# Performance work log

Measured on AMD Instinct MI355X. Metric: run time of the kernel, lower is better.

The kernel has to match this reference:

```python
import jax, jax.numpy as jnp
import numpy as np

N_EMBED = 1024
N_HEAD = 16
HEAD_SIZE = N_EMBED // N_HEAD  # 64
SEQ = 2048
BATCH = 2
EPS = 1e-5


def setup_inputs() -> dict:
    key = jax.random.key(0)
    ks = jax.random.split(key, 16)
    s = lambda fan_in: 1.0 / np.sqrt(fan_in)
    d, h, hs, f = N_EMBED, N_HEAD, HEAD_SIZE, 4 * N_EMBED
    return {
        "x": jax.random.normal(ks[0], (BATCH, SEQ, d), dtype=jnp.float32),
        # per-head QKV projections (no bias), stacked over heads: [H, D, hs]
        "wq": jax.random.normal(ks[1], (h, d, hs), dtype=jnp.float32) * s(d),
        "wk": jax.random.normal(ks[2], (h, d, hs), dtype=jnp.float32) * s(d),
        "wv": jax.random.normal(ks[3], (h, d, hs), dtype=jnp.float32) * s(d),
        "w_proj": jax.random.normal(ks[4], (d, d), dtype=jnp.float32) * s(d),
        "b_proj": jnp.zeros((d,), dtype=jnp.float32),
        "w1": jax.random.normal(ks[5], (d, f), dtype=jnp.float32) * s(d),
        "b1": jnp.zeros((f,), dtype=jnp.float32),
        "w2": jax.random.normal(ks[6], (f, d), dtype=jnp.float32) * s(f),
        "b2": jnp.zeros((d,), dtype=jnp.float32),
        "g1": jnp.ones((d,), dtype=jnp.float32),
        "be1": jnp.zeros((d,), dtype=jnp.float32),
        "g2": jnp.ones((d,), dtype=jnp.float32),
        "be2": jnp.zeros((d,), dtype=jnp.float32),
    }


def _layer_norm(x, gamma, beta):
    mu = jnp.mean(x, axis=-1, keepdims=True)
    var = jnp.mean(jnp.square(x - mu), axis=-1, keepdims=True)
    return (x - mu) * jax.lax.rsqrt(var + EPS) * gamma + beta


def reference(x, wq, wk, wv, w_proj, b_proj, w1, b1, w2, b2, g1, be1, g2, be2):
    B, S, D = x.shape
    # per-head projections (vectorized over heads): [B, H, S, hs]
    q = jnp.einsum("bsd,hdk->bhsk", x, wq)
    k = jnp.einsum("bsd,hdk->bhsk", x, wk)
    v = jnp.einsum("bsd,hdk->bhsk", x, wv)
    scale = HEAD_SIZE ** -0.5
    scores = jnp.einsum("bhsk,bhtk->bhst", q, k) * scale  # [B,H,S,S]
    causal = jnp.tril(jnp.ones((S, S), dtype=bool))
    scores = jnp.where(causal, scores, -jnp.inf)
    w = jax.nn.softmax(scores, axis=-1)  # dropout=0 -> identity
    attn = jnp.einsum("bhst,bhtk->bhsk", w, v)  # [B,H,S,hs]
    # concat heads (head-major ordering matches torch.cat over heads)
    attn = attn.transpose(0, 2, 1, 3).reshape(B, S, D)
    y = attn @ w_proj + b_proj
    x = _layer_norm(x + y, g1, be1)
    y = jax.nn.relu(x @ w1 + b1) @ w2 + b2
    x = _layer_norm(x + y, g2, be2)
    return x
```

## Files before the change

kernel.cpp:

```cpp
#include <hip/hip_runtime.h>


typedef unsigned short u16;
typedef unsigned int u32;
typedef __attribute__((ext_vector_type(8))) short bf16x8;
typedef __attribute__((ext_vector_type(4))) float f32x4;
typedef __attribute__((ext_vector_type(2))) u32 u32x2;
typedef __attribute__((ext_vector_type(4))) _Float16 f16x4;

#define MFMA16(a, b, c) __builtin_amdgcn_mfma_f32_16x16x32_bf16(a, b, c, 0, 0, 0)
#define MFMAH(a, b, c) __builtin_amdgcn_mfma_f32_16x16x16f16(a, b, c, 0, 0, 0)

__device__ __forceinline__ u16 f2b(float f) {
  unsigned int u = __builtin_bit_cast(unsigned int, f);
  u = (u + 0x7fffu + ((u >> 16) & 1u)) >> 16;
  return (u16)u;
}

__device__ __forceinline__ void gload_lds16(const u16* g, u16* l) {
  __builtin_amdgcn_global_load_lds((const __attribute__((address_space(1))) void*)g,
                                   (__attribute__((address_space(3))) void*)l, 16, 0, 0);
}

__device__ __forceinline__ u32 pkrtz(float lo, float hi) {
  return __builtin_bit_cast(u32, __builtin_amdgcn_cvt_pkrtz(lo, hi));
}

__device__ __forceinline__ f16x4 pack4h(float a, float b, float c, float d) {
  u32x2 r = {pkrtz(a, b), pkrtz(c, d)};
  return __builtin_bit_cast(f16x4, r);
}

__device__ __forceinline__ u16 f2h(float v) {
  return __builtin_bit_cast(u16, (_Float16)v);
}


__global__ __launch_bounds__(256) void pack_all(
    const float* __restrict__ x, const float* __restrict__ wq,
    const float* __restrict__ wk, const float* __restrict__ wv,
    const float* __restrict__ wp, const float* __restrict__ w1,
    const float* __restrict__ w2, u16* __restrict__ Xbf, u16* __restrict__ WqkvT,
    u16* __restrict__ WprojT, u16* __restrict__ W1T, u16* __restrict__ W2T) {
  int bid = blockIdx.x;
  int t = threadIdx.x;
  if (bid >= 12288) {
    size_t i = ((size_t)(bid - 12288) * 256 + t) * 4;
    float4 v = *(const float4*)(x + i);
    Xbf[i + 0] = f2b(v.x);
    Xbf[i + 1] = f2b(v.y);
    Xbf[i + 2] = f2b(v.z);
    Xbf[i + 3] = f2b(v.w);
    return;
  }
  __shared__ float tile[32][33];
  int tx = t & 31, ty = t >> 5;
  const float* src;
  u16* dst;
  int R, C, r0, c0;
  float scale = 1.0f;
  if (bid < 3072) {
    int z = bid >> 6, q = bid & 63;
    int p = z >> 4, h = z & 15;
    src = (p == 0 ? wq : (p == 1 ? wk : wv)) + (size_t)h * 1024 * 64;
    scale = (p == 0) ? 0.1803368801f : 1.0f;
    dst = WqkvT + (size_t)(p * 1024 + h * 64) * 1024;
    R = 1024; C = 64;
    c0 = (q & 1) * 32; r0 = (q >> 1) * 32;
  } else if (bid < 4096) {
    int q = bid - 3072;
    src = wp; dst = WprojT; R = 1024; C = 1024;
    c0 = (q & 31) * 32; r0 = (q >> 5) * 32;
  } else if (bid < 8192) {
    int q = bid - 4096;
    src = w1; dst = W1T; R = 1024; C = 4096;
    c0 = (q & 127) * 32; r0 = (q >> 7) * 32;
  } else {
    int q = bid - 8192;
    src = w2; dst = W2T; R = 4096; C = 1024;
    c0 = (q & 31) * 32; r0 = (q >> 5) * 32;
  }
#pragma unroll
  for (int i = 0; i < 4; ++i)
    tile[ty + i * 8][tx] = src[(size_t)(r0 + ty + i * 8) * C + c0 + tx];
  __syncthreads();
#pragma unroll
  for (int i = 0; i < 4; ++i)
    dst[(size_t)(c0 + ty + i * 8) * R + r0 + tx] = f2b(tile[tx][ty + i * 8] * scale);
}


template <int MODE>
__global__ __launch_bounds__(256, 4) void gemm_bf16(const u16* __restrict__ A,
                                                    const u16* __restrict__ Bt, int M,
                                                    int N, int Kc, int lda,
                                                    const float* __restrict__ bias,
                                                    u16* __restrict__ outB, int ldc,
                                                    u16* __restrict__ vtg) {
  constexpr int BM = 128, BN = 128, BK = 64;
  constexpr int IM = 4, JN = 4;
  __shared__ u16 As[BM * BK];
  __shared__ u16 Bs[BN * BK];
  int t = threadIdx.x;
  int m0 = blockIdx.x * BM, n0 = blockIdx.y * BN;
  int kb = blockIdx.z * Kc;
  int lane = t & 63, wid = t >> 6;
  int wm = (wid >> 1) * 64, wn = (wid & 1) * 64;
  int m16 = lane & 15, quad = lane >> 4;
  int sw = m16 & 7;

  f32x4 acc[IM][JN] = {};

  for (int k0 = kb; k0 < kb + Kc; k0 += BK) {
    __syncthreads();
#pragma unroll
    for (int i = 0; i < 4; ++i) {
      int S = i * 256 + t;
      int row = S >> 3, c = S & 7;
      gload_lds16(&A[(size_t)(m0 + row) * lda + k0 + (c ^ (row & 7)) * 8],
                  &As[(i * 256 + wid * 64) * 8]);
    }
#pragma unroll
    for (int i = 0; i < 4; ++i) {
      int S = i * 256 + t;
      int row = S >> 3, c = S & 7;
      gload_lds16(&Bt[(size_t)(n0 + row) * lda + k0 + (c ^ (row & 7)) * 8],
                  &Bs[(i * 256 + wid * 64) * 8]);
    }
    __syncthreads();
#pragma unroll
    for (int kk = 0; kk < 2; ++kk) {
      bf16x8 af[IM], bfr[JN];
      int slot = (kk * 4 + quad) ^ sw;
#pragma unroll
      for (int i = 0; i < IM; ++i)
        af[i] = *(const bf16x8*)&As[(wm + i * 16 + m16) * BK + slot * 8];
#pragma unroll
      for (int j = 0; j < JN; ++j)
        bfr[j] = *(const bf16x8*)&Bs[(wn + j * 16 + m16) * BK + slot * 8];
#pragma unroll
      for (int i = 0; i < IM; ++i)
#pragma unroll
        for (int j = 0; j < JN; ++j) acc[i][j] = MFMA16(af[i], bfr[j], acc[i][j]);
    }
  }

  if (MODE == 3 && n0 >= 2048) {
#pragma unroll
    for (int i = 0; i < IM; ++i)
#pragma unroll
      for (int j = 0; j < JN; ++j) {
        int dg = n0 + wn + j * 16 + m16 - 2048;
        int hh = dg >> 6, dd = dg & 63;
        int token = m0 + wm + i * 16 + quad * 4;
        int bb = token >> 11, tt = token & 2047;
        u32x2 pv = {pkrtz(acc[i][j][0], acc[i][j][1]),
                    pkrtz(acc[i][j][2], acc[i][j][3])};
        *(u32x2*)&vtg[(((size_t)bb * 16 + hh) * 64 + dd) * 2048 + tt] = pv;
      }
    return;
  }

  u16* pb = (MODE == 4) ? outB + (size_t)blockIdx.z * M * N : outB;
#pragma unroll
  for (int i = 0; i < IM; ++i)
#pragma unroll
    for (int j = 0; j < JN; ++j) {
      int col = n0 + wn + j * 16 + m16;
      float bv = (MODE == 1) ? bias[col] : 0.0f;
#pragma unroll
      for (int r = 0; r < 4; ++r) {
        int row = m0 + wm + i * 16 + quad * 4 + r;
        float v = acc[i][j][r];
        if (MODE == 1) {
          v += bv;
          v = v > 0.0f ? v : 0.0f;
          pb[(size_t)row * ldc + col] = f2b(v);
        } else if (MODE == 4) {
          pb[(size_t)row * ldc + col] = f2h(v);
        } else {
          pb[(size_t)row * ldc + col] = f2b(v);
        }
      }
    }
}


template <int MODE>
__global__ __launch_bounds__(512) void gemm8(const u16* __restrict__ A,
                                             const u16* __restrict__ Bt, int M, int N,
                                             int Kc, int lda,
                                             const float* __restrict__ bias,
                                             u16* __restrict__ outB, int ldc) {
  __shared__ __align__(16) u16 As[2][2][128 * 64];
  __shared__ __align__(16) u16 Bs[2][2][128 * 64];
  int t = threadIdx.x;
  int lane = t & 63, wid = t >> 6;
  int m16 = lane & 15, quad = lane >> 4, sw = m16 & 7;
  int wr = wid >> 2, wc = wid & 3;
  int m0 = blockIdx.x * 256, n0 = blockIdx.y * 256;
  int kb = blockIdx.z * Kc;
  int NT = Kc >> 6;

  int ahalf = t >> 8;
  int at = t & 255;
  int aw = wid & 3;
  int brow0 = (wc & 1) * 64;

  f32x4 acc[8][4] = {};
  bf16x8 afc[2][2], afn[2][2], bfc[4][2], bfn[4][2];

#define STAGE_B(bf, bh, kt)                                                        \
  {                                                                                \
    _Pragma("unroll") for (int l = 0; l < 2; ++l) {                                \
      int slot = l * 512 + t;                                                      \
      int row = slot >> 3, c = slot & 7;                                           \
      gload_lds16(&Bt[(size_t)(n0 + (bh)*128 + row) * lda + kb + (kt)*64 +         \
                      (c ^ (row & 7)) * 8],                                        \
                  &Bs[bf][bh][(l * 512 + wid * 64) * 8]);                          \
    }                                                                              \
  }

#define STAGE_A(bf, qp, kt)                                                        \
  {                                                                                \
    _Pragma("unroll") for (int l = 0; l < 2; ++l) {                                \
      int slot = l * 256 + at;                                                     \
      int row = slot >> 3, c = slot & 7;                                           \
      int lrow = (qp)*64 + row;                                                    \
      gload_lds16(&A[(size_t)(m0 + ahalf * 128 + lrow) * lda + kb + (kt)*64 +      \
                     (c ^ (row & 7)) * 8],                                         \
                  &As[bf][ahalf][((qp)*512 + l * 256 + aw * 64) * 8]);             \
    }                                                                              \
  }

#define READ_AF(dst, base, qdv)                                                    \
  {                                                                                \
    _Pragma("unroll") for (int mi = 0; mi < 2; ++mi)                               \
        _Pragma("unroll") for (int kk = 0; kk < 2; ++kk)                           \
            dst[mi][kk] = *(const bf16x8*)&(base)[((qdv)*32 + mi * 16 + m16) * 64 +\
                                                  ((kk * 4 + quad) ^ sw) * 8];     \
  }

#define READ_BF(dst, base)                                                         \
  {                                                                                \
    _Pragma("unroll") for (int j = 0; j < 4; ++j)                                  \
        _Pragma("unroll") for (int kk = 0; kk < 2; ++kk)                           \
            dst[j][kk] = *(const bf16x8*)&(base)[(brow0 + j * 16 + m16) * 64 +     \
                                                 ((kk * 4 + quad) ^ sw) * 8];      \
  }

  STAGE_B(0, 0, 0);
  STAGE_B(0, 1, 0);
  STAGE_A(0, 0, 0);
  STAGE_A(0, 1, 0);
  if (NT > 1) {
    STAGE_B(1, 0, 1);
    STAGE_B(1, 1, 1);
    STAGE_A(1, 0, 1);
    asm volatile("s_waitcnt vmcnt(6)" ::: "memory");
  } else {
    asm volatile("s_waitcnt vmcnt(0)" ::: "memory");
  }
  __builtin_amdgcn_s_barrier();
  asm volatile("" ::: "memory");
  READ_BF(bfc, &Bs[0][wc >> 1][0]);
  READ_AF(afc, &As[0][wr][0], 0);

  for (int kt = 0; kt < NT; ++kt) {
    int buf = kt & 1;
    const u16* Ab = &As[buf][wr][0];
    const u16* Abn = &As[buf ^ 1][wr][0];
    const u16* Bbn = &Bs[buf ^ 1][wc >> 1][0];
#pragma unroll
    for (int qd = 0; qd < 4; ++qd) {
      if (qd < 3) {
        READ_AF(afn, Ab, qd + 1);
      } else if (kt + 1 < NT) {
        READ_BF(bfn, Bbn);
        READ_AF(afn, Abn, 0);
      }
      if (qd == 0) {
        if (kt + 1 < NT) STAGE_A(buf ^ 1, 1, kt + 1);
      } else if (qd == 1) {
        if (kt + 2 < NT) STAGE_B(buf, 0, kt + 2);
      } else if (qd == 2) {
        if (kt + 2 < NT) STAGE_B(buf, 1, kt + 2);
      } else {
        if (kt + 2 < NT) STAGE_A(buf, 0, kt + 2);
      }
      if (qd < 3)
        asm volatile("s_waitcnt lgkmcnt(4)" ::: "memory");
      else if (kt + 1 < NT)
        asm volatile("s_waitcnt lgkmcnt(12)" ::: "memory");
      else
        asm volatile("s_waitcnt lgkmcnt(0)" ::: "memory");
      __builtin_amdgcn_sched_barrier(0);
      __builtin_amdgcn_s_setprio(1);
#pragma unroll
      for (int mi = 0; mi < 2; ++mi)
#pragma unroll
        for (int j = 0; j < 4; ++j)
#pragma unroll
          for (int kk = 0; kk < 2; ++kk)
            acc[qd * 2 + mi][j] = MFMA16(afc[mi][kk], bfc[j][kk], acc[qd * 2 + mi][j]);
      __builtin_amdgcn_s_setprio(0);
      if (qd == 0) {
        if (kt + 1 < NT)
          asm volatile("s_waitcnt vmcnt(8)" ::: "memory");
        else
          asm volatile("s_waitcnt vmcnt(0)" ::: "memory");
      } else if (qd == 2) {
        if (kt + 2 < NT)
          asm volatile("s_waitcnt vmcnt(6)" ::: "memory");
        else
          asm volatile("s_waitcnt vmcnt(0)" ::: "memory");
      }
      if (qd < 3 || kt + 1 < NT) {
#pragma unroll
        for (int mi = 0; mi < 2; ++mi)
#pragma unroll
          for (int kk = 0; kk < 2; ++kk) afc[mi][kk] = afn[mi][kk];
        if (qd == 3) {
#pragma unroll
          for (int j = 0; j < 4; ++j)
#pragma unroll
            for (int kk = 0; kk < 2; ++kk) bfc[j][kk] = bfn[j][kk];
        }
      }
      asm volatile("" ::: "memory");
      __builtin_amdgcn_s_barrier();
      asm volatile("" ::: "memory");
    }
  }

  u16* pb = (MODE == 4) ? outB + (size_t)blockIdx.z * M * N : outB;
#pragma unroll
  for (int mf = 0; mf < 8; ++mf)
#pragma unroll
    for (int j = 0; j < 4; ++j) {
      int col = n0 + wc * 64 + j * 16 + m16;
      float bv = (MODE == 1) ? bias[col] : 0.0f;
#pragma unroll
      for (int r = 0; r < 4; ++r) {
        int row = m0 + wr * 128 + mf * 16 + quad * 4 + r;
        float v = acc[mf][j][r];
        if (MODE == 1) {
          v += bv;
          v = v > 0.0f ? v : 0.0f;
          pb[(size_t)row * ldc + col] = f2b(v);
        } else {
          pb[(size_t)row * ldc + col] = f2h(v);
        }
      }
    }
#undef STAGE_B
#undef STAGE_A
#undef READ_AF
#undef READ_BF
}


__constant__ unsigned char R_QB[40] = {
    15, 15, 15, 15, 14, 14, 11, 11, 11, 10, 7,  7,  3,
    14, 14, 13, 13, 13, 13, 12, 12, 10, 10, 9,  9,  6,  6,
    12, 12, 9,  8,  8,  8,  5,  5,  2,
    4,  4,  1,  0};
__constant__ unsigned char R_K0[40] = {
    0,  8,  16, 24, 0,  8,  0,  8,  16, 0,  0,  8,  0,
    16, 23, 0,  7,  14, 21, 0,  7,  8,  15, 0,  7,  0,  7,
    14, 20, 14, 0,  6,  12, 0,  6,  0,
    0,  5,  0,  0};
__constant__ unsigned char R_NIT[40] = {
    8, 8, 8, 8, 8, 8, 8, 8, 8, 8, 8, 8, 8,
    7, 7, 7, 7, 7, 7, 7, 7, 7, 7, 7, 7, 7, 7,
    6, 6, 6, 6, 6, 6, 6, 6, 6,
    5, 5, 4, 2};
__constant__ unsigned char R_ST[40] = {
    32, 33, 34, 35, 28, 29, 17, 18, 19, 14, 6,  7,  255,
    30, 31, 24, 25, 26, 27, 20, 21, 15, 16, 11, 12, 4,  5,
    22, 23, 13, 8,  9,  10, 2,  3,  255,
    0,  1,  255, 255};
__constant__ unsigned char CB_BASE[12] = {0, 2, 4, 6, 8, 11, 14, 17, 20, 24, 28, 32};

__global__ __launch_bounds__(256) void attn_part(const u16* __restrict__ qk,
                                                 const u16* __restrict__ vtg,
                                                 u16* __restrict__ attn_out,
                                                 u16* __restrict__ opart0,
                                                 u16* __restrict__ opart1,
                                                 float2* __restrict__ ml) {
  int rank = blockIdx.x >> 5, bh = blockIdx.x & 31;
  int qb = R_QB[rank];
  int k_start = R_K0[rank] * 64;
  int iters = R_NIT[rank];
  int st = R_ST[rank];
  int b = bh >> 4, h = bh & 15;

  int t = threadIdx.x, lane = t & 63, w = t >> 6;
  int m16 = lane & 15, quad = lane >> 4;
  int wq0 = qb * 128 + w * 32;

  __shared__ u16 Ks[2][64 * 64];
  __shared__ u16 Vs[2][64 * 64];

  bf16x8 qa[2][2];
#pragma unroll
  for (int qs = 0; qs < 2; ++qs) {
    const u16* qp = qk + (size_t)(b * 2048 + wq0 + qs * 16 + m16) * 2048 + h * 64;
    qa[qs][0] = *(const bf16x8*)&qp[quad * 8];
    qa[qs][1] = *(const bf16x8*)&qp[32 + quad * 8];
  }

  f32x4 oT[2][4] = {};
  f32x4 oL[2] = {};
  const f16x4 ones = {(_Float16)1.0f, (_Float16)1.0f, (_Float16)1.0f, (_Float16)1.0f};

  int row0 = t >> 3, c0 = t & 7;
  int row1 = 32 + row0;
  const u16* kbase = qk + (size_t)(b * 2048) * 2048 + 1024 + h * 64;
  const u16* vbase = vtg + ((size_t)(b * 16 + h) * 64) * 2048;
  int sw = m16 & 7;

#define STAGE_ASYNC(T0, BUF)                                                        \
  {                                                                                 \
    gload_lds16(&kbase[(size_t)((T0) + row0) * 2048 + (c0 ^ (row0 & 7)) * 8],       \
                &Ks[BUF][(w * 64) * 8]);                                            \
    gload_lds16(&kbase[(size_t)((T0) + row1) * 2048 + (c0 ^ (row1 & 7)) * 8],       \
                &Ks[BUF][(256 + w * 64) * 8]);                                      \
    gload_lds16(&vbase[(size_t)row0 * 2048 + (T0) + (c0 ^ (row0 & 7)) * 8],         \
                &Vs[BUF][(w * 64) * 8]);                                            \
    gload_lds16(&vbase[(size_t)row1 * 2048 + (T0) + (c0 ^ (row1 & 7)) * 8],         \
                &Vs[BUF][(256 + w * 64) * 8]);                                      \
  }

  STAGE_ASYNC(k_start, 0);
  __syncthreads();

  for (int it = 0; it < iters; ++it) {
    int t0 = k_start + it * 64;
    int cur = it & 1;
    if (it + 1 < iters) STAGE_ASYNC(t0 + 64, !cur);

    if (t0 <= wq0 + 31) {
      f32x4 sv[2][4];
      __builtin_amdgcn_s_setprio(1);
#pragma unroll
      for (int ts = 0; ts < 4; ++ts) {
        bf16x8 ka0 = *(const bf16x8*)&Ks[cur][(ts * 16 + m16) * 64 + (quad ^ sw) * 8];
        bf16x8 ka1 =
            *(const bf16x8*)&Ks[cur][(ts * 16 + m16) * 64 + ((4 + quad) ^ sw) * 8];
#pragma unroll
        for (int qs = 0; qs < 2; ++qs) {
          f32x4 a = {};
          a = MFMA16(ka0, qa[qs][0], a);
          a = MFMA16(ka1, qa[qs][1], a);
          sv[qs][ts] = a;
        }
      }
      __builtin_amdgcn_s_setprio(0);
      if (t0 + 63 > wq0) {
#pragma unroll
        for (int qs = 0; qs < 2; ++qs)
#pragma unroll
          for (int ts = 0; ts < 4; ++ts)
#pragma unroll
            for (int rr = 0; rr < 4; ++rr) {
              int key = t0 + ts * 16 + quad * 4 + rr;
              if (key > wq0 + qs * 16 + m16) sv[qs][ts][rr] = -3e38f;
            }
      }
      f16x4 pf[2][4];
#pragma unroll
      for (int qs = 0; qs < 2; ++qs)
#pragma unroll
        for (int ts = 0; ts < 4; ++ts) {
          float p0 = exp2f(sv[qs][ts][0] - 8.0f);
          float p1 = exp2f(sv[qs][ts][1] - 8.0f);
          float p2 = exp2f(sv[qs][ts][2] - 8.0f);
          float p3 = exp2f(sv[qs][ts][3] - 8.0f);
          pf[qs][ts] = pack4h(p0, p1, p2, p3);
        }
      __builtin_amdgcn_s_setprio(1);
#pragma unroll
      for (int ts = 0; ts < 4; ++ts) {
        oL[0] = MFMAH(ones, pf[0][ts], oL[0]);
        oL[1] = MFMAH(ones, pf[1][ts], oL[1]);
#pragma unroll
        for (int ds = 0; ds < 4; ++ds) {
          f16x4 av = __builtin_bit_cast(
              f16x4, *(const u32x2*)&Vs[cur][(ds * 16 + m16) * 64 +
                                             (((ts * 2 + (quad >> 1)) ^ sw) * 8) +
                                             (quad & 1) * 4]);
          oT[0][ds] = MFMAH(av, pf[0][ts], oT[0][ds]);
          oT[1][ds] = MFMAH(av, pf[1][ts], oT[1][ds]);
        }
      }
      __builtin_amdgcn_s_setprio(0);
    }
    __syncthreads();
  }
#undef STAGE_ASYNC

  if (st == 255) {
#pragma unroll
    for (int qs = 0; qs < 2; ++qs) {
      float rl = 1.0f / oL[qs][0];
      int q = wq0 + qs * 16 + m16;
#pragma unroll
      for (int ds = 0; ds < 4; ++ds) {
        f32x4 o = oT[qs][ds];
        u32x2 ov = {(u32)f2b(o[0] * rl) | ((u32)f2b(o[1] * rl) << 16),
                    (u32)f2b(o[2] * rl) | ((u32)f2b(o[3] * rl) << 16)};
        *(u32x2*)&attn_out[(size_t)(b * 2048 + q) * 1024 + h * 64 + ds * 16 +
                           quad * 4] = ov;
      }
    }
  } else {
    u16* po;
    size_t sb;
    if (st < 32) {
      po = opart0;
      sb = ((size_t)st * 32 + bh) * 128;
    } else {
      po = opart1;
      sb = ((size_t)(st - 32) * 32 + bh) * 128;
    }
    size_t mlb = ((size_t)st * 32 + bh) * 128;
#pragma unroll
    for (int qs = 0; qs < 2; ++qs) {
      float ls = oL[qs][0];
      int qloc = w * 32 + qs * 16 + m16;
#pragma unroll
      for (int ds = 0; ds < 4; ++ds) {
        f32x4 o = oT[qs][ds];
        u32x2 ov = {pkrtz(o[0], o[1]), pkrtz(o[2], o[3])};
        *(u32x2*)&po[(sb + qloc) * 64 + ds * 16 + quad * 4] = ov;
      }
      if (quad == 0) ml[mlb + qloc] = make_float2(0.0f, ls);
    }
  }
}

__global__ __launch_bounds__(256) void attn_comb(const u16* __restrict__ opart0,
                                                 const u16* __restrict__ opart1,
                                                 const float2* __restrict__ ml,
                                                 u16* __restrict__ attn_out) {
  int qb = 4 + blockIdx.x, bh = blockIdx.y;
  int b = bh >> 4, h = bh & 15;
  int nseg = (qb < 8) ? 2 : (qb < 12 ? 3 : 4);
  int base = CB_BASE[qb - 4];
  int t = threadIdx.x;
  int q = t >> 1, dh = (t & 1) * 32;

  float lsum = 0.0f;
  for (int s = 0; s < nseg; ++s)
    lsum += ml[((size_t)(base + s) * 32 + bh) * 128 + q].y;
  float rl = 1.0f / lsum;

  constexpr size_t SLOT = (size_t)32 * 128 * 64;
  const u16* orow[4];
  for (int s = 0; s < nseg; ++s) {
    int sa = base + s;
    const u16* bp =
        (sa < 32) ? opart0 + (size_t)sa * SLOT : opart1 + (size_t)(sa - 32) * SLOT;
    orow[s] = bp + ((size_t)bh * 128 + q) * 64 + dh;
  }

  size_t oout = (size_t)(b * 2048 + qb * 128 + q) * 1024 + h * 64 + dh;
#pragma unroll 2
  for (int dd = 0; dd < 32; dd += 4) {
    float o0 = 0, o1 = 0, o2 = 0, o3 = 0;
    for (int s = 0; s < nseg; ++s) {
      f16x4 hv = __builtin_bit_cast(f16x4, *(const u32x2*)&orow[s][dd]);
      o0 += (float)hv[0];
      o1 += (float)hv[1];
      o2 += (float)hv[2];
      o3 += (float)hv[3];
    }
    u32x2 ov = {(u32)f2b(o0 * rl) | ((u32)f2b(o1 * rl) << 16),
                (u32)f2b(o2 * rl) | ((u32)f2b(o3 * rl) << 16)};
    *(u32x2*)&attn_out[oout + dd] = ov;
  }
}


__global__ __launch_bounds__(256) void ln_comb(const u16* __restrict__ parts, int np,
                                               const float* __restrict__ bias,
                                               const float* __restrict__ resid,
                                               const float* __restrict__ g,
                                               const float* __restrict__ be,
                                               float* __restrict__ outF,
                                               u16* __restrict__ outB) {
  int row = blockIdx.x;
  int t = threadIdx.x;
  size_t off = (size_t)row * 1024 + t * 4;
  float4 bv4 = *(const float4*)(bias + t * 4);
  float a0 = bv4.x, a1 = bv4.y, a2 = bv4.z, a3 = bv4.w;
  for (int c = 0; c < np; ++c) {
    f16x4 hv =
        __builtin_bit_cast(f16x4, *(const u32x2*)&parts[(size_t)c * 4096 * 1024 + off]);
    a0 += (float)hv[0];
    a1 += (float)hv[1];
    a2 += (float)hv[2];
    a3 += (float)hv[3];
  }
  float4 rv = *(const float4*)(resid + off);
  a0 += rv.x;
  a1 += rv.y;
  a2 += rv.z;
  a3 += rv.w;

  float s = a0 + a1 + a2 + a3;
  float sq = a0 * a0 + a1 * a1 + a2 * a2 + a3 * a3;
#pragma unroll
  for (int d = 1; d < 64; d <<= 1) {
    s += __shfl_xor(s, d);
    sq += __shfl_xor(sq, d);
  }
  __shared__ float red[8];
  int lane = t & 63, wid = t >> 6;
  if (lane == 0) {
    red[wid] = s;
    red[4 + wid] = sq;
  }
  __syncthreads();
  s = red[0] + red[1] + red[2] + red[3];
  sq = red[4] + red[5] + red[6] + red[7];
  float mu = s * (1.0f / 1024.0f);
  float var = sq * (1.0f / 1024.0f) - mu * mu;
  float rstd = rsqrtf(var + 1e-5f);
  float4 gv = *(const float4*)(g + t * 4);
  float4 bev = *(const float4*)(be + t * 4);
  float o0 = (a0 - mu) * rstd * gv.x + bev.x;
  float o1 = (a1 - mu) * rstd * gv.y + bev.y;
  float o2 = (a2 - mu) * rstd * gv.z + bev.z;
  float o3 = (a3 - mu) * rstd * gv.w + bev.w;
  if (outF) {
    float4 ov = {o0, o1, o2, o3};
    *(float4*)(outF + off) = ov;
  }
  if (outB) {
    outB[off + 0] = f2b(o0);
    outB[off + 1] = f2b(o1);
    outB[off + 2] = f2b(o2);
    outB[off + 3] = f2b(o3);
  }
}


extern "C" void kernel_launch(void* const* d_in, const int* in_sizes, int n_in,
                              void* d_out, int out_size, void* d_ws, size_t ws_size,
                              hipStream_t stream) {
  const float* x = (const float*)d_in[0];
  const float* wq = (const float*)d_in[1];
  const float* wk = (const float*)d_in[2];
  const float* wv = (const float*)d_in[3];
  const float* w_proj = (const float*)d_in[4];
  const float* b_proj = (const float*)d_in[5];
  const float* w1 = (const float*)d_in[6];
  const float* b1 = (const float*)d_in[7];
  const float* w2 = (const float*)d_in[8];
  const float* b2 = (const float*)d_in[9];
  const float* g1 = (const float*)d_in[10];
  const float* be1 = (const float*)d_in[11];
  const float* g2 = (const float*)d_in[12];
  const float* be2 = (const float*)d_in[13];
  float* out = (float*)d_out;

  const int M = 4096;
  char* w = (char*)d_ws;
  u16* Xbf = (u16*)w;        w += (size_t)M * 1024 * 2;
  u16* WqkvT = (u16*)w;      w += (size_t)3072 * 1024 * 2;
  u16* WprojT = (u16*)w;     w += (size_t)1024 * 1024 * 2;
  u16* W1T = (u16*)w;        w += (size_t)4096 * 1024 * 2;
  u16* X1b = (u16*)w;        w += (size_t)M * 1024 * 2;
  u16* W2T = (u16*)w;        w += (size_t)1024 * 4096 * 2;
  u16* QK = (u16*)w;         w += (size_t)M * 2048 * 2;
  u16* Vtg = (u16*)w;        w += (size_t)2 * 16 * 64 * 2048 * 2;
  u16* Attn = (u16*)w;       w += (size_t)M * 1024 * 2;
  float* X1f = (float*)w;    w += (size_t)M * 1024 * 4;

  u16* Pdown = Xbf;
  u16* Pproj = QK;
  u16* Hbuf = QK;
  u16* Opart0 = (u16*)X1f;
  u16* Opart1 = Xbf;
  float2* Ml = (float2*)((char*)d_ws + (size_t)4 * 1024 * 1024);

  pack_all<<<16384, 256, 0, stream>>>(x, wq, wk, wv, w_proj, w1, w2, Xbf, WqkvT,
                                      WprojT, W1T, W2T);

  gemm_bf16<3><<<dim3(32, 24, 1), 256, 0, stream>>>(Xbf, WqkvT, M, 3072, 1024, 1024,
                                                    nullptr, QK, 2048, Vtg);

  attn_part<<<1280, 256, 0, stream>>>(QK, Vtg, Attn, Opart0, Opart1, Ml);
  attn_comb<<<dim3(12, 32), 256, 0, stream>>>(Opart0, Opart1, Ml, Attn);

  gemm_bf16<4><<<dim3(32, 8, 2), 256, 0, stream>>>(Attn, WprojT, M, 1024, 512, 1024,
                                                   nullptr, Pproj, 1024, nullptr);
  ln_comb<<<M, 256, 0, stream>>>(Pproj, 2, b_proj, x, g1, be1, X1f, X1b);

  gemm8<1><<<dim3(16, 16, 1), 512, 0, stream>>>(X1b, W1T, M, 4096, 1024, 1024, b1,
                                                Hbuf, 4096);

  gemm_bf16<4><<<dim3(32, 8, 4), 256, 0, stream>>>(Hbuf, W2T, M, 1024, 1024, 4096,
                                                   nullptr, Pdown, 1024, nullptr);
  ln_comb<<<M, 256, 0, stream>>>(Pdown, 4, b2, X1f, g2, be2, out, nullptr);
}
```

Measured before the change: 365.1 us.

## Stage V-transpose through LDS, trim gemm8 registers, rebalance attention split schedule

After: 331.1 us. 1.1x faster.

```diff
diff --git a/kernel.cpp b/kernel.cpp
--- a/kernel.cpp
+++ b/kernel.cpp
@@ -6,6 +6,7 @@
 typedef __attribute__((ext_vector_type(8))) short bf16x8;
 typedef __attribute__((ext_vector_type(4))) float f32x4;
 typedef __attribute__((ext_vector_type(2))) u32 u32x2;
+typedef __attribute__((ext_vector_type(4))) u32 u32x4;
 typedef __attribute__((ext_vector_type(4))) _Float16 f16x4;
 
 #define MFMA16(a, b, c) __builtin_amdgcn_mfma_f32_16x16x32_bf16(a, b, c, 0, 0, 0)
@@ -99,8 +100,9 @@
                                                     u16* __restrict__ vtg) {
   constexpr int BM = 128, BN = 128, BK = 64;
   constexpr int IM = 4, JN = 4;
-  __shared__ u16 As[BM * BK];
-  __shared__ u16 Bs[BN * BK];
+  __shared__ u16 Smem[2][BM * BK];
+  u16* const As = &Smem[0][0];
+  u16* const Bs = &Smem[1][0];
   int t = threadIdx.x;
   int m0 = blockIdx.x * BM, n0 = blockIdx.y * BN;
   int kb = blockIdx.z * Kc;
@@ -146,18 +148,30 @@
   }
 
   if (MODE == 3 && n0 >= 2048) {
+    u16* const Ts = &Smem[0][0];
+    __syncthreads();
 #pragma unroll
     for (int i = 0; i < IM; ++i)
 #pragma unroll
       for (int j = 0; j < JN; ++j) {
-        int dg = n0 + wn + j * 16 + m16 - 2048;
-        int hh = dg >> 6, dd = dg & 63;
-        int token = m0 + wm + i * 16 + quad * 4;
-        int bb = token >> 11, tt = token & 2047;
+        int dgl = wn + j * 16 + m16;
+        int tl0 = wm + i * 16 + quad * 4;
         u32x2 pv = {pkrtz(acc[i][j][0], acc[i][j][1]),
                     pkrtz(acc[i][j][2], acc[i][j][3])};
-        *(u32x2*)&vtg[(((size_t)bb * 16 + hh) * 64 + dd) * 2048 + tt] = pv;
-      }
+        int ch = tl0 >> 3, off = tl0 & 7;
+        *(u32x2*)&Ts[dgl * 128 + ((ch ^ (dgl & 15)) << 3) + off] = pv;
+      }
+    __syncthreads();
+    int bb = m0 >> 11, tt0 = m0 & 2047;
+    int lane16 = t & 15;
+#pragma unroll
+    for (int it = 0; it < 8; ++it) {
+      int row = it * 16 + (t >> 4);
+      u32x4 v = *(const u32x4*)&Ts[row * 128 + ((lane16 ^ (row & 15)) << 3)];
+      int dgg = n0 - 2048 + row;
+      int hh = dgg >> 6, dd = dgg & 63;
+      *(u32x4*)&vtg[(((size_t)bb * 16 + hh) * 64 + dd) * 2048 + tt0 + lane16 * 8] = v;
+    }
     return;
   }
 
@@ -187,11 +201,11 @@
 
 
 template <int MODE>
-__global__ __launch_bounds__(512) void gemm8(const u16* __restrict__ A,
-                                             const u16* __restrict__ Bt, int M, int N,
-                                             int Kc, int lda,
-                                             const float* __restrict__ bias,
-                                             u16* __restrict__ outB, int ldc) {
+__global__ __launch_bounds__(512, 2) void gemm8(const u16* __restrict__ A,
+                                                const u16* __restrict__ Bt, int M, int N,
+                                                int Kc, int lda,
+                                                const float* __restrict__ bias,
+                                                u16* __restrict__ outB, int ldc) {
   __shared__ __align__(16) u16 As[2][2][128 * 64];
   __shared__ __align__(16) u16 Bs[2][2][128 * 64];
   int t = threadIdx.x;
@@ -208,7 +222,7 @@
   int brow0 = (wc & 1) * 64;
 
   f32x4 acc[8][4] = {};
-  bf16x8 afc[2][2], afn[2][2], bfc[4][2], bfn[4][2];
+  bf16x8 afc[2][2], afn[2][2], bfc[4][2];
 
 #define STAGE_B(bf, bh, kt)                                                        \
   {                                                                                \
@@ -276,7 +290,6 @@
       if (qd < 3) {
         READ_AF(afn, Ab, qd + 1);
       } else if (kt + 1 < NT) {
-        READ_BF(bfn, Bbn);
         READ_AF(afn, Abn, 0);
       }
       if (qd == 0) {
@@ -288,10 +301,8 @@
       } else {
         if (kt + 2 < NT) STAGE_A(buf, 0, kt + 2);
       }
-      if (qd < 3)
+      if (qd < 3 || kt + 1 < NT)
         asm volatile("s_waitcnt lgkmcnt(4)" ::: "memory");
-      else if (kt + 1 < NT)
-        asm volatile("s_waitcnt lgkmcnt(12)" ::: "memory");
       else
         asm volatile("s_waitcnt lgkmcnt(0)" ::: "memory");
       __builtin_amdgcn_sched_barrier(0);
@@ -304,6 +315,7 @@
           for (int kk = 0; kk < 2; ++kk)
             acc[qd * 2 + mi][j] = MFMA16(afc[mi][kk], bfc[j][kk], acc[qd * 2 + mi][j]);
       __builtin_amdgcn_s_setprio(0);
+      if (qd == 3 && kt + 1 < NT) READ_BF(bfc, Bbn);
       if (qd == 0) {
         if (kt + 1 < NT)
           asm volatile("s_waitcnt vmcnt(8)" ::: "memory");
@@ -320,12 +332,6 @@
         for (int mi = 0; mi < 2; ++mi)
 #pragma unroll
           for (int kk = 0; kk < 2; ++kk) afc[mi][kk] = afn[mi][kk];
-        if (qd == 3) {
-#pragma unroll
-          for (int j = 0; j < 4; ++j)
-#pragma unroll
-            for (int kk = 0; kk < 2; ++kk) bfc[j][kk] = bfn[j][kk];
-        }
       }
       asm volatile("" ::: "memory");
       __builtin_amdgcn_s_barrier();
@@ -360,33 +366,24 @@
 }
 
 
-__constant__ unsigned char R_QB[40] = {
-    15, 15, 15, 15, 14, 14, 11, 11, 11, 10, 7,  7,  3,
-    14, 14, 13, 13, 13, 13, 12, 12, 10, 10, 9,  9,  6,  6,
-    12, 12, 9,  8,  8,  8,  5,  5,  2,
-    4,  4,  1,  0};
-__constant__ unsigned char R_K0[40] = {
-    0,  8,  16, 24, 0,  8,  0,  8,  16, 0,  0,  8,  0,
-    16, 23, 0,  7,  14, 21, 0,  7,  8,  15, 0,  7,  0,  7,
-    14, 20, 14, 0,  6,  12, 0,  6,  0,
-    0,  5,  0,  0};
-__constant__ unsigned char R_NIT[40] = {
-    8, 8, 8, 8, 8, 8, 8, 8, 8, 8, 8, 8, 8,
-    7, 7, 7, 7, 7, 7, 7, 7, 7, 7, 7, 7, 7, 7,
-    6, 6, 6, 6, 6, 6, 6, 6, 6,
-    5, 5, 4, 2};
-__constant__ unsigned char R_ST[40] = {
-    32, 33, 34, 35, 28, 29, 17, 18, 19, 14, 6,  7,  255,
-    30, 31, 24, 25, 26, 27, 20, 21, 15, 16, 11, 12, 4,  5,
-    22, 23, 13, 8,  9,  10, 2,  3,  255,
-    0,  1,  255, 255};
-__constant__ unsigned char CB_BASE[12] = {0, 2, 4, 6, 8, 11, 14, 17, 20, 24, 28, 32};
+__constant__ unsigned char R_QB[30] = {
+    5, 11, 11, 10, 10, 15, 15, 4, 9, 9, 13, 14, 14, 14, 15,
+    8, 8, 12, 12, 13, 13, 3, 7, 7, 12, 6, 6, 2, 1, 0};
+__constant__ unsigned char R_K0[30] = {
+    0, 0, 12, 0, 11, 0, 11, 0, 0, 10, 0, 0, 10, 20, 22,
+    0, 9, 0, 9, 10, 19, 0, 0, 8, 18, 0, 7, 0, 0, 0};
+__constant__ unsigned char R_NIT[30] = {
+    12, 12, 12, 11, 11, 11, 11, 10, 10, 10, 10, 10, 10, 10, 10,
+    9, 9, 9, 9, 9, 9, 8, 8, 8, 8, 7, 7, 6, 4, 2};
+__constant__ unsigned char R_ST[30] = {
+    255, 10, 11, 8, 9, 21, 22, 255, 6, 7, 15, 18, 19, 20, 23,
+    4, 5, 12, 13, 16, 17, 255, 2, 3, 14, 0, 1, 255, 255, 255};
+__constant__ unsigned char CB_BASE[10] = {0, 2, 4, 6, 8, 10, 12, 15, 18, 21};
 
 __global__ __launch_bounds__(256) void attn_part(const u16* __restrict__ qk,
                                                  const u16* __restrict__ vtg,
                                                  u16* __restrict__ attn_out,
-                                                 u16* __restrict__ opart0,
-                                                 u16* __restrict__ opart1,
+                                                 u16* __restrict__ opart,
                                                  float2* __restrict__ ml) {
   int rank = blockIdx.x >> 5, bh = blockIdx.x & 31;
   int qb = R_QB[rank];
@@ -515,16 +512,7 @@
       }
     }
   } else {
-    u16* po;
-    size_t sb;
-    if (st < 32) {
-      po = opart0;
-      sb = ((size_t)st * 32 + bh) * 128;
-    } else {
-      po = opart1;
-      sb = ((size_t)(st - 32) * 32 + bh) * 128;
-    }
-    size_t mlb = ((size_t)st * 32 + bh) * 128;
+    size_t sb = ((size_t)st * 32 + bh) * 128;
 #pragma unroll
     for (int qs = 0; qs < 2; ++qs) {
       float ls = oL[qs][0];
@@ -533,21 +521,20 @@
       for (int ds = 0; ds < 4; ++ds) {
         f32x4 o = oT[qs][ds];
         u32x2 ov = {pkrtz(o[0], o[1]), pkrtz(o[2], o[3])};
-        *(u32x2*)&po[(sb + qloc) * 64 + ds * 16 + quad * 4] = ov;
-      }
-      if (quad == 0) ml[mlb + qloc] = make_float2(0.0f, ls);
-    }
-  }
-}
-
-__global__ __launch_bounds__(256) void attn_comb(const u16* __restrict__ opart0,
-                                                 const u16* __restrict__ opart1,
+        *(u32x2*)&opart[(sb + qloc) * 64 + ds * 16 + quad * 4] = ov;
+      }
+      if (quad == 0) ml[sb + qloc] = make_float2(0.0f, ls);
+    }
+  }
+}
+
+__global__ __launch_bounds__(256) void attn_comb(const u16* __restrict__ opart,
                                                  const float2* __restrict__ ml,
                                                  u16* __restrict__ attn_out) {
-  int qb = 4 + blockIdx.x, bh = blockIdx.y;
+  int qb = 6 + blockIdx.x, bh = blockIdx.y;
   int b = bh >> 4, h = bh & 15;
-  int nseg = (qb < 8) ? 2 : (qb < 12 ? 3 : 4);
-  int base = CB_BASE[qb - 4];
+  int nseg = (qb < 12) ? 2 : 3;
+  int base = CB_BASE[qb - 6];
   int t = threadIdx.x;
   int q = t >> 1, dh = (t & 1) * 32;
 
@@ -557,13 +544,9 @@
   float rl = 1.0f / lsum;
 
   constexpr size_t SLOT = (size_t)32 * 128 * 64;
-  const u16* orow[4];
-  for (int s = 0; s < nseg; ++s) {
-    int sa = base + s;
-    const u16* bp =
-        (sa < 32) ? opart0 + (size_t)sa * SLOT : opart1 + (size_t)(sa - 32) * SLOT;
-    orow[s] = bp + ((size_t)bh * 128 + q) * 64 + dh;
-  }
+  const u16* orow[3];
+  for (int s = 0; s < nseg; ++s)
+    orow[s] = opart + (size_t)(base + s) * SLOT + ((size_t)bh * 128 + q) * 64 + dh;
 
   size_t oout = (size_t)(b * 2048 + qb * 128 + q) * 1024 + h * 64 + dh;
 #pragma unroll 2
@@ -682,8 +665,7 @@
   u16* Pdown = Xbf;
   u16* Pproj = QK;
   u16* Hbuf = QK;
-  u16* Opart0 = (u16*)X1f;
-  u16* Opart1 = Xbf;
+  u16* Opart = (u16*)X1f;
   float2* Ml = (float2*)((char*)d_ws + (size_t)4 * 1024 * 1024);
 
   pack_all<<<16384, 256, 0, stream>>>(x, wq, wk, wv, w_proj, w1, w2, Xbf, WqkvT,
@@ -692,8 +674,8 @@
   gemm_bf16<3><<<dim3(32, 24, 1), 256, 0, stream>>>(Xbf, WqkvT, M, 3072, 1024, 1024,
                                                     nullptr, QK, 2048, Vtg);
 
-  attn_part<<<1280, 256, 0, stream>>>(QK, Vtg, Attn, Opart0, Opart1, Ml);
-  attn_comb<<<dim3(12, 32), 256, 0, stream>>>(Opart0, Opart1, Ml, Attn);
+  attn_part<<<960, 256, 0, stream>>>(QK, Vtg, Attn, Opart, Ml);
+  attn_comb<<<dim3(10, 32), 256, 0, stream>>>(Opart, Ml, Attn);
 
   gemm_bf16<4><<<dim3(32, 8, 2), 256, 0, stream>>>(Attn, WprojT, M, 1024, 512, 1024,
                                                    nullptr, Pproj, 1024, nullptr);
```
